# Kernel optimization log

Measured on AMD Instinct MI355X. Metric: run time of the kernel, lower is better.

Reference implementation:

```python
import jax, jax.numpy as jnp
import numpy as np

B, L, C, H = 4, 1024, 768, 12
D = C // H  # head_ch = 64


def setup_inputs() -> dict:
    key = jax.random.key(0)
    ks = jax.random.split(key, 8)
    s = 1.0 / np.sqrt(C)
    return {
        "inputs_q": jax.random.normal(ks[0], (B, L, C), jnp.float32),
        "inputs_kv": jax.random.normal(ks[1], (B, L, C), jnp.float32),
        "Wq": jax.random.normal(ks[2], (C, H * D), jnp.float32) * s,
        "Wk": jax.random.normal(ks[3], (C, H * D), jnp.float32) * s,
        "Wv": jax.random.normal(ks[4], (C, H * D), jnp.float32) * s,
        "Wout": jax.random.normal(ks[5], (H * D, C), jnp.float32) * s,
        "W_pre": jax.random.normal(ks[6], (H, H), jnp.float32) * (1.0 / np.sqrt(H)),
        "W_post": jax.random.normal(ks[7], (H, H), jnp.float32) * (1.0 / np.sqrt(H)),
    }


def reference(inputs_q, inputs_kv, Wq, Wk, Wv, Wout, W_pre, W_post):
    # Linear projections (no bias), split into heads: b l (h d) -> b h l d
    def split_heads(x):
        b, l, _ = x.shape
        return x.reshape(b, l, H, D).transpose(0, 2, 1, 3)

    q = split_heads(inputs_q @ Wq) / jnp.sqrt(jnp.asarray(D, inputs_q.dtype))
    k = split_heads(inputs_kv @ Wk)
    v = split_heads(inputs_kv @ Wv)

    # Attention logits [b, h, l, k]
    weights = jnp.einsum('bhld,bhkd->bhlk', q, k)
    # Talking-heads: learned cross-head mixing pre-softmax
    weights = jnp.einsum('bhlk,hi->bilk', weights, W_pre)
    weights = jax.nn.softmax(weights, axis=-1)
    # Talking-heads post-softmax mixing
    weights = jnp.einsum('bhlk,hi->bilk', weights, W_post)

    scores = jnp.einsum('bhlk,bhkd->bhld', weights, v)
    scores = scores.transpose(0, 2, 1, 3).reshape(B, L, H * D)  # b l (h d)
    return scores @ Wout
```

## Files before the change

kernel.cpp:

```cpp
#include <hip/hip_runtime.h>

#define BB 4
#define LL 1024
#define CC 768
#define HH 12
#define DD 64

typedef unsigned short ushort_t;
typedef __attribute__((ext_vector_type(8))) short bf16x8;
typedef __attribute__((ext_vector_type(4))) float f32x4;
typedef __attribute__((ext_vector_type(2))) float f32x2;

__device__ inline ushort_t f2bf(float x) {
    union { float f; unsigned u; } v; v.f = x;
    unsigned r = (v.u + 0x7FFFu + ((v.u >> 16) & 1u)) >> 16;
    return (ushort_t)r;
}
__device__ inline float bf2f(ushort_t u) {
    union { unsigned u; float f; } v; v.u = ((unsigned)u) << 16;
    return v.f;
}
__device__ inline float u2f(unsigned u) {
    union { unsigned u; float f; } v; v.u = u;
    return v.f;
}

__device__ inline void stage_rows(const ushort_t* __restrict__ g, int stride,
                                  ushort_t* lds, int nbytes, int wave, int lane) {
    const int ko = (lane & 3) << 3;
    const int rsub = lane >> 2;
    for (int off = wave * 1024; off < nbytes; off += 4096) {
        int row = (off >> 6) + rsub;
        __builtin_amdgcn_global_load_lds(
            (const __attribute__((address_space(1))) void*)(g + (size_t)row * stride + ko),
            (__attribute__((address_space(3))) void*)(lds + (off >> 1)),
            16, 0, 0);
    }
}

__global__ __launch_bounds__(256) void prep(const float* __restrict__ q, const float* __restrict__ kv,
                                            const float* __restrict__ w0, const float* __restrict__ w1,
                                            const float* __restrict__ w2, const float* __restrict__ w3,
                                            ushort_t* __restrict__ qo, ushort_t* __restrict__ kvo,
                                            ushort_t* __restrict__ o0, ushort_t* __restrict__ o1,
                                            ushort_t* __restrict__ o2, ushort_t* __restrict__ o3) {
    __shared__ float t[32][33];
    const int bx = blockIdx.x;
    if (bx < 3072) {
        const float* src = bx < 1536 ? q : kv;
        ushort_t* dst = bx < 1536 ? qo : kvo;
        int bb = bx < 1536 ? bx : bx - 1536;
        size_t i = ((size_t)bb * 256 + threadIdx.x) * 8;
        float4 a = *(const float4*)(src + i);
        float4 b = *(const float4*)(src + i + 4);
        ushort_t u[8] = {f2bf(a.x), f2bf(a.y), f2bf(a.z), f2bf(a.w),
                         f2bf(b.x), f2bf(b.y), f2bf(b.z), f2bf(b.w)};
        *(uint4*)(dst + i) = *(uint4*)u;
    } else {
        int w = bx - 3072;
        int z = w / 576, rem = w % 576;
        const float* W = z == 0 ? w0 : z == 1 ? w1 : z == 2 ? w2 : w3;
        ushort_t* Wt   = z == 0 ? o0 : z == 1 ? o1 : z == 2 ? o2 : o3;
        const int c = threadIdx.x & 31, r0 = threadIdx.x >> 5;
        const int kb = (rem / 24) * 32, nb = (rem % 24) * 32;
#pragma unroll
        for (int i = 0; i < 4; ++i)
            t[r0 + 8 * i][c] = W[(size_t)(kb + r0 + 8 * i) * CC + nb + c];
        __syncthreads();
#pragma unroll
        for (int i = 0; i < 4; ++i)
            Wt[(size_t)(nb + r0 + 8 * i) * CC + kb + c] = f2bf(t[c][r0 + 8 * i]);
    }
}

__global__ __launch_bounds__(256) void proj_gemm(const ushort_t* __restrict__ Aq,
                                                 const ushort_t* __restrict__ Akv,
                                                 const ushort_t* __restrict__ Wqt,
                                                 const ushort_t* __restrict__ Wkt,
                                                 const ushort_t* __restrict__ Wvt,
                                                 ushort_t* __restrict__ Qo,
                                                 ushort_t* __restrict__ Ko,
                                                 ushort_t* __restrict__ Vto) {
    const int z = blockIdx.z;
    const ushort_t* A  = (z == 0) ? Aq : Akv;
    const ushort_t* Wt = (z == 0) ? Wqt : (z == 1 ? Wkt : Wvt);

    __shared__ __align__(16) ushort_t a_lds[128 * 32];
    __shared__ __align__(16) ushort_t b_lds[128 * 32];

    const int tid = threadIdx.x;
    const int bm = blockIdx.x * 128, bn = blockIdx.y * 128;
    const int wave = tid >> 6, lane = tid & 63;
    const int quad = lane >> 4, lq = lane & 15;
    const int wr = wave >> 1, wc = wave & 1;

    f32x4 acc[4][4] = {};

    for (int k0 = 0; k0 < CC; k0 += 32) {
        stage_rows(A + (size_t)bm * CC + k0, CC, a_lds, 8192, wave, lane);
        stage_rows(Wt + (size_t)bn * CC + k0, CC, b_lds, 8192, wave, lane);
        __syncthreads();
        bf16x8 af[4], bfr[4];
#pragma unroll
        for (int mi = 0; mi < 4; ++mi)
            af[mi] = *(bf16x8*)&a_lds[(wr * 64 + mi * 16 + lq) * 32 + quad * 8];
#pragma unroll
        for (int ni = 0; ni < 4; ++ni)
            bfr[ni] = *(bf16x8*)&b_lds[(wc * 64 + ni * 16 + lq) * 32 + quad * 8];
#pragma unroll
        for (int mi = 0; mi < 4; ++mi)
#pragma unroll
            for (int ni = 0; ni < 4; ++ni)
                acc[mi][ni] = __builtin_amdgcn_mfma_f32_16x16x32_bf16(af[mi], bfr[ni], acc[mi][ni], 0, 0, 0);
        __syncthreads();
    }

    const float scale = (z == 0) ? 0.125f : 1.0f;
#pragma unroll
    for (int mi = 0; mi < 4; ++mi)
#pragma unroll
        for (int ni = 0; ni < 4; ++ni)
#pragma unroll
            for (int r = 0; r < 4; ++r) {
                int row = bm + wr * 64 + mi * 16 + quad * 4 + r;
                int col = bn + wc * 64 + ni * 16 + lq;
                int b = row >> 10, l = row & 1023, h = col >> 6, d = col & 63;
                ushort_t v = f2bf(acc[mi][ni][r] * scale);
                if (z == 0)      Qo[((size_t)(b * HH + h) * LL + l) * DD + d] = v;
                else if (z == 1) Ko[((size_t)(b * HH + h) * LL + l) * DD + d] = v;
                else             Vto[((size_t)(b * HH + h) * DD + d) * LL + l] = v;
            }
}

__global__ __launch_bounds__(256) void qk_gemm(const ushort_t* __restrict__ Q,
                                               const ushort_t* __restrict__ K,
                                               ushort_t* __restrict__ S) {
    __shared__ __align__(16) ushort_t a_lds[128 * 32];
    __shared__ __align__(16) ushort_t b_lds[128 * 32];

    const int tid = threadIdx.x;
    const int bm = blockIdx.x * 128, bn = blockIdx.y * 128;
    const int bh = blockIdx.z;
    const ushort_t* Qh = Q + (size_t)bh * LL * DD;
    const ushort_t* Kh = K + (size_t)bh * LL * DD;
    const int wave = tid >> 6, lane = tid & 63;
    const int quad = lane >> 4, lq = lane & 15;
    const int wr = wave >> 1, wc = wave & 1;

    f32x4 acc[4][4] = {};

    for (int k0 = 0; k0 < DD; k0 += 32) {
        stage_rows(Qh + (size_t)bm * DD + k0, DD, a_lds, 8192, wave, lane);
        stage_rows(Kh + (size_t)bn * DD + k0, DD, b_lds, 8192, wave, lane);
        __syncthreads();
        bf16x8 af[4], bfr[4];
#pragma unroll
        for (int mi = 0; mi < 4; ++mi)
            af[mi] = *(bf16x8*)&a_lds[(wr * 64 + mi * 16 + lq) * 32 + quad * 8];
#pragma unroll
        for (int ni = 0; ni < 4; ++ni)
            bfr[ni] = *(bf16x8*)&b_lds[(wc * 64 + ni * 16 + lq) * 32 + quad * 8];
#pragma unroll
        for (int mi = 0; mi < 4; ++mi)
#pragma unroll
            for (int ni = 0; ni < 4; ++ni)
                acc[mi][ni] = __builtin_amdgcn_mfma_f32_16x16x32_bf16(af[mi], bfr[ni], acc[mi][ni], 0, 0, 0);
        __syncthreads();
    }

#pragma unroll
    for (int mi = 0; mi < 4; ++mi)
#pragma unroll
        for (int ni = 0; ni < 4; ++ni)
#pragma unroll
            for (int r = 0; r < 4; ++r) {
                int row = bm + wr * 64 + mi * 16 + quad * 4 + r;
                int col = bn + wc * 64 + ni * 16 + lq;
                S[((size_t)bh * LL + row) * LL + col] = f2bf(acc[mi][ni][r]);
            }
}

__global__ __launch_bounds__(256) void mix_softmax(ushort_t* __restrict__ S,
                                                   const float* __restrict__ Wpre,
                                                   const float* __restrict__ Wpost) {
    __shared__ float reds[4][16];

    const int tid = threadIdx.x;
    const int wave = tid >> 6, lane = tid & 63;
    const int l = blockIdx.x, b = blockIdx.y;

    const size_t hstride = (size_t)LL * LL;
    const size_t base = ((size_t)(b * HH) * LL + l) * LL + tid * 4;

    f32x2 p[HH][2];
#pragma unroll
    for (int i = 0; i < HH; ++i) { p[i][0] = 0.f; p[i][1] = 0.f; }
#pragma unroll
    for (int h = 0; h < HH; ++h) {
        uint2 raw = *(const uint2*)&S[base + h * hstride];
        f32x2 v0, v1;
        v0.x = u2f(raw.x << 16); v0.y = u2f(raw.x & 0xFFFF0000u);
        v1.x = u2f(raw.y << 16); v1.y = u2f(raw.y & 0xFFFF0000u);
#pragma unroll
        for (int i = 0; i < HH; ++i) {
            float w = Wpre[h * HH + i];
            p[i][0] += v0 * w;
            p[i][1] += v1 * w;
        }
    }

    float sm[HH];
#pragma unroll
    for (int i = 0; i < HH; ++i) {
        p[i][0].x = __expf(p[i][0].x); p[i][0].y = __expf(p[i][0].y);
        p[i][1].x = __expf(p[i][1].x); p[i][1].y = __expf(p[i][1].y);
        f32x2 t2 = p[i][0] + p[i][1];
        float ss = t2.x + t2.y;
#pragma unroll
        for (int off = 32; off; off >>= 1) ss += __shfl_xor(ss, off);
        sm[i] = ss;
    }
    if (lane == 0) {
#pragma unroll
        for (int i = 0; i < HH; ++i) reds[wave][i] = sm[i];
    }
    __syncthreads();
#pragma unroll
    for (int i = 0; i < HH; ++i) {
        float tot = (reds[0][i] + reds[1][i]) + (reds[2][i] + reds[3][i]);
        float inv = 1.0f / tot;
        p[i][0] *= inv; p[i][1] *= inv;
    }

#pragma unroll
    for (int i = 0; i < HH; ++i) {
        f32x2 a0 = 0.f, a1 = 0.f;
#pragma unroll
        for (int h = 0; h < HH; ++h) {
            float w = Wpost[h * HH + i];
            a0 += p[h][0] * w;
            a1 += p[h][1] * w;
        }
        ushort_t u[4] = {f2bf(a0.x), f2bf(a0.y), f2bf(a1.x), f2bf(a1.y)};
        *(uint2*)&S[base + i * hstride] = *(uint2*)u;
    }
}

__global__ __launch_bounds__(256) void pv_gemm(const ushort_t* __restrict__ P,
                                               const ushort_t* __restrict__ Vt,
                                               ushort_t* __restrict__ att) {
    __shared__ __align__(16) ushort_t a_lds[64 * 32];
    __shared__ __align__(16) ushort_t b_lds[64 * 32];

    const int tid = threadIdx.x;
    const int bm = blockIdx.x * 64;
    const int bh = blockIdx.y;
    const int b = bh / HH, ih = bh % HH;
    const ushort_t* Ph = P + ((size_t)bh << 20);
    const ushort_t* Vh = Vt + (size_t)bh * LL * DD;
    const int wave = tid >> 6, lane = tid & 63;
    const int quad = lane >> 4, lq = lane & 15;
    const int wr = wave >> 1, wc = wave & 1;

    f32x4 acc[2][2] = {};

    for (int k0 = 0; k0 < LL; k0 += 32) {
        stage_rows(Ph + (size_t)bm * LL + k0, LL, a_lds, 4096, wave, lane);
        stage_rows(Vh + k0, LL, b_lds, 4096, wave, lane);
        __syncthreads();
        bf16x8 af[2], bfr[2];
#pragma unroll
        for (int mi = 0; mi < 2; ++mi)
            af[mi] = *(bf16x8*)&a_lds[(wr * 32 + mi * 16 + lq) * 32 + quad * 8];
#pragma unroll
        for (int ni = 0; ni < 2; ++ni)
            bfr[ni] = *(bf16x8*)&b_lds[(wc * 32 + ni * 16 + lq) * 32 + quad * 8];
#pragma unroll
        for (int mi = 0; mi < 2; ++mi)
#pragma unroll
            for (int ni = 0; ni < 2; ++ni)
                acc[mi][ni] = __builtin_amdgcn_mfma_f32_16x16x32_bf16(af[mi], bfr[ni], acc[mi][ni], 0, 0, 0);
        __syncthreads();
    }

#pragma unroll
    for (int mi = 0; mi < 2; ++mi)
#pragma unroll
        for (int ni = 0; ni < 2; ++ni)
#pragma unroll
            for (int r = 0; r < 4; ++r) {
                int lrow = bm + wr * 32 + mi * 16 + quad * 4 + r;
                int col = wc * 32 + ni * 16 + lq;
                att[((size_t)(b * LL) + lrow) * CC + ih * DD + col] = f2bf(acc[mi][ni][r]);
            }
}

__global__ __launch_bounds__(256) void out_gemm(const ushort_t* __restrict__ A,
                                                const ushort_t* __restrict__ Wt,
                                                float* __restrict__ out) {
    __shared__ __align__(16) ushort_t a_lds[128 * 32];
    __shared__ __align__(16) ushort_t b_lds[64 * 32];

    const int tid = threadIdx.x;
    const int bm = blockIdx.x * 128, bn = blockIdx.y * 64;
    const int wave = tid >> 6, lane = tid & 63;
    const int quad = lane >> 4, lq = lane & 15;
    const int wr = wave >> 1, wc = wave & 1;

    f32x4 acc[4][2] = {};

    for (int k0 = 0; k0 < CC; k0 += 32) {
        stage_rows(A + (size_t)bm * CC + k0, CC, a_lds, 8192, wave, lane);
        stage_rows(Wt + (size_t)bn * CC + k0, CC, b_lds, 4096, wave, lane);
        __syncthreads();
        bf16x8 af[4], bfr[2];
#pragma unroll
        for (int mi = 0; mi < 4; ++mi)
            af[mi] = *(bf16x8*)&a_lds[(wr * 64 + mi * 16 + lq) * 32 + quad * 8];
#pragma unroll
        for (int ni = 0; ni < 2; ++ni)
            bfr[ni] = *(bf16x8*)&b_lds[(wc * 32 + ni * 16 + lq) * 32 + quad * 8];
#pragma unroll
        for (int mi = 0; mi < 4; ++mi)
#pragma unroll
            for (int ni = 0; ni < 2; ++ni)
                acc[mi][ni] = __builtin_amdgcn_mfma_f32_16x16x32_bf16(af[mi], bfr[ni], acc[mi][ni], 0, 0, 0);
        __syncthreads();
    }

#pragma unroll
    for (int mi = 0; mi < 4; ++mi)
#pragma unroll
        for (int ni = 0; ni < 2; ++ni)
#pragma unroll
            for (int r = 0; r < 4; ++r) {
                int row = bm + wr * 64 + mi * 16 + quad * 4 + r;
                int col = bn + wc * 32 + ni * 16 + lq;
                out[(size_t)row * CC + col] = acc[mi][ni][r];
            }
}

extern "C" void kernel_launch(void* const* d_in, const int* in_sizes, int n_in,
                              void* d_out, int out_size, void* d_ws, size_t ws_size,
                              hipStream_t stream) {
    const float* inputs_q  = (const float*)d_in[0];
    const float* inputs_kv = (const float*)d_in[1];
    const float* Wq   = (const float*)d_in[2];
    const float* Wk   = (const float*)d_in[3];
    const float* Wv   = (const float*)d_in[4];
    const float* Wout = (const float*)d_in[5];
    const float* Wpre  = (const float*)d_in[6];
    const float* Wpost = (const float*)d_in[7];
    float* out = (float*)d_out;

    const size_t nS   = (size_t)BB * HH * LL * LL;
    const size_t nQKV = (size_t)BB * HH * LL * DD;
    const size_t nW   = (size_t)CC * CC;

    ushort_t* Sb   = (ushort_t*)d_ws;
    ushort_t* Qb   = Sb + nS;
    ushort_t* Kb   = Qb + nQKV;
    ushort_t* Vtb  = Kb + nQKV;
    ushort_t* attb = Vtb + nQKV;
    ushort_t* inq  = attb + nQKV;
    ushort_t* inkv = inq + nQKV;
    ushort_t* Wqt  = inkv + nQKV;
    ushort_t* Wkt  = Wqt + nW;
    ushort_t* Wvt  = Wkt + nW;
    ushort_t* Wot  = Wvt + nW;

    dim3 blk(256);

    prep<<<dim3(5376), blk, 0, stream>>>(inputs_q, inputs_kv, Wq, Wk, Wv, Wout,
                                         inq, inkv, Wqt, Wkt, Wvt, Wot);
    proj_gemm<<<dim3(32, 6, 3), blk, 0, stream>>>(inq, inkv, Wqt, Wkt, Wvt, Qb, Kb, Vtb);
    qk_gemm<<<dim3(8, 8, BB * HH), blk, 0, stream>>>(Qb, Kb, Sb);
    mix_softmax<<<dim3(LL, BB), blk, 0, stream>>>(Sb, Wpre, Wpost);
    pv_gemm<<<dim3(16, BB * HH), blk, 0, stream>>>(Sb, Vtb, attb);
    out_gemm<<<dim3(32, 12), blk, 0, stream>>>(attb, Wot, out);
}
```

Baseline: 233.7 us.

## Fuse QK with pre-mix/exp and PV with post-mix, dropping separate softmax pass

The QK GEMM now computes all 12 heads for a 32x32 tile, applies the pre-softmax head mixing and exp in registers, and writes head-interleaved exp values plus atomically accumulated row sums Z. A new PV kernel reads those values, normalises by 1/Z, applies post-softmax mixing on the fly, and runs the PV MFMAs from swizzled LDS tiles. This removes the standalone mix_softmax kernel and one full read-modify-write of the score tensor. In exchange it skips max-subtraction in softmax, which risks overflow, and it adds float atomics for Z, zeroed in prep.

```diff
diff --git a/kernel.cpp b/kernel.cpp
--- a/kernel.cpp
+++ b/kernel.cpp
@@ -1,4 +1,5 @@
 #include <hip/hip_runtime.h>
+#include <hip/hip_bf16.h>
 
 #define BB 4
 #define LL 1024
@@ -16,13 +17,14 @@
     unsigned r = (v.u + 0x7FFFu + ((v.u >> 16) & 1u)) >> 16;
     return (ushort_t)r;
 }
-__device__ inline float bf2f(ushort_t u) {
-    union { unsigned u; float f; } v; v.u = ((unsigned)u) << 16;
-    return v.f;
-}
 __device__ inline float u2f(unsigned u) {
     union { unsigned u; float f; } v; v.u = u;
     return v.f;
+}
+__device__ inline unsigned pack2bf(float lo, float hi) {
+    union { __hip_bfloat162 v; unsigned u; } r;
+    r.v = __float22bfloat162_rn(make_float2(lo, hi));
+    return r.u;
 }
 
 __device__ inline void stage_rows(const ushort_t* __restrict__ g, int stride,
@@ -43,7 +45,8 @@
                                             const float* __restrict__ w2, const float* __restrict__ w3,
                                             ushort_t* __restrict__ qo, ushort_t* __restrict__ kvo,
                                             ushort_t* __restrict__ o0, ushort_t* __restrict__ o1,
-                                            ushort_t* __restrict__ o2, ushort_t* __restrict__ o3) {
+                                            ushort_t* __restrict__ o2, ushort_t* __restrict__ o3,
+                                            float* __restrict__ Zp) {
     __shared__ float t[32][33];
     const int bx = blockIdx.x;
     if (bx < 3072) {
@@ -56,7 +59,7 @@
         ushort_t u[8] = {f2bf(a.x), f2bf(a.y), f2bf(a.z), f2bf(a.w),
                          f2bf(b.x), f2bf(b.y), f2bf(b.z), f2bf(b.w)};
         *(uint4*)(dst + i) = *(uint4*)u;
-    } else {
+    } else if (bx < 5376) {
         int w = bx - 3072;
         int z = w / 576, rem = w % 576;
         const float* W = z == 0 ? w0 : z == 1 ? w1 : z == 2 ? w2 : w3;
@@ -70,6 +73,8 @@
 #pragma unroll
         for (int i = 0; i < 4; ++i)
             Wt[(size_t)(nb + r0 + 8 * i) * CC + kb + c] = f2bf(t[c][r0 + 8 * i]);
+    } else {
+        Zp[(bx - 5376) * 256 + threadIdx.x] = 0.f;
     }
 }
 
@@ -132,167 +137,191 @@
             }
 }
 
-__global__ __launch_bounds__(256) void qk_gemm(const ushort_t* __restrict__ Q,
-                                               const ushort_t* __restrict__ K,
-                                               ushort_t* __restrict__ S) {
-    __shared__ __align__(16) ushort_t a_lds[128 * 32];
-    __shared__ __align__(16) ushort_t b_lds[128 * 32];
+__global__ __launch_bounds__(256) void qk_premix(const ushort_t* __restrict__ Q,
+                                                 const ushort_t* __restrict__ K,
+                                                 const float* __restrict__ Wpre,
+                                                 ushort_t* __restrict__ E,
+                                                 float* __restrict__ Z) {
+    __shared__ __align__(16) ushort_t k_lds[2][2048];
+    __shared__ __align__(16) ushort_t q_lds[2][2048];
 
     const int tid = threadIdx.x;
-    const int bm = blockIdx.x * 128, bn = blockIdx.y * 128;
-    const int bh = blockIdx.z;
-    const ushort_t* Qh = Q + (size_t)bh * LL * DD;
-    const ushort_t* Kh = K + (size_t)bh * LL * DD;
-    const int wave = tid >> 6, lane = tid & 63;
+    const int bk = blockIdx.x * 32;
+    const int bl = blockIdx.y * 32;
+    const int b  = blockIdx.z;
+    const int lane = tid & 63, wave = tid >> 6;
     const int quad = lane >> 4, lq = lane & 15;
     const int wr = wave >> 1, wc = wave & 1;
 
-    f32x4 acc[4][4] = {};
-
-    for (int k0 = 0; k0 < DD; k0 += 32) {
-        stage_rows(Qh + (size_t)bm * DD + k0, DD, a_lds, 8192, wave, lane);
-        stage_rows(Kh + (size_t)bn * DD + k0, DD, b_lds, 8192, wave, lane);
-        __syncthreads();
-        bf16x8 af[4], bfr[4];
-#pragma unroll
-        for (int mi = 0; mi < 4; ++mi)
-            af[mi] = *(bf16x8*)&a_lds[(wr * 64 + mi * 16 + lq) * 32 + quad * 8];
-#pragma unroll
-        for (int ni = 0; ni < 4; ++ni)
-            bfr[ni] = *(bf16x8*)&b_lds[(wc * 64 + ni * 16 + lq) * 32 + quad * 8];
-#pragma unroll
-        for (int mi = 0; mi < 4; ++mi)
-#pragma unroll
-            for (int ni = 0; ni < 4; ++ni)
-                acc[mi][ni] = __builtin_amdgcn_mfma_f32_16x16x32_bf16(af[mi], bfr[ni], acc[mi][ni], 0, 0, 0);
-        __syncthreads();
-    }
-
-#pragma unroll
-    for (int mi = 0; mi < 4; ++mi)
-#pragma unroll
-        for (int ni = 0; ni < 4; ++ni)
-#pragma unroll
-            for (int r = 0; r < 4; ++r) {
-                int row = bm + wr * 64 + mi * 16 + quad * 4 + r;
-                int col = bn + wc * 64 + ni * 16 + lq;
-                S[((size_t)bh * LL + row) * LL + col] = f2bf(acc[mi][ni][r]);
+    const int o = tid << 4;
+    const int goff = ((o >> 6) & 31) * DD + (o >> 11) * 32 + ((o >> 4) & 3) * 8;
+    const ushort_t* Kbase = K + ((size_t)b * HH * LL + bk) * DD;
+    const ushort_t* Qbase = Q + ((size_t)b * HH * LL + bl) * DD;
+
+    f32x4 acc[HH] = {};
+
+#define STAGE_QK(h, bf)                                                                             \
+    do {                                                                                            \
+        __builtin_amdgcn_global_load_lds(                                                           \
+            (const __attribute__((address_space(1))) void*)(Kbase + (size_t)(h) * LL * DD + goff),  \
+            (__attribute__((address_space(3))) void*)(&k_lds[bf][0] + (o >> 1)), 16, 0, 0);         \
+        __builtin_amdgcn_global_load_lds(                                                           \
+            (const __attribute__((address_space(1))) void*)(Qbase + (size_t)(h) * LL * DD + goff),  \
+            (__attribute__((address_space(3))) void*)(&q_lds[bf][0] + (o >> 1)), 16, 0, 0);         \
+    } while (0)
+
+    STAGE_QK(0, 0);
+    __syncthreads();
+#pragma unroll
+    for (int h = 0; h < HH; ++h) {
+        const int buf = h & 1;
+        if (h < HH - 1) STAGE_QK(h + 1, buf ^ 1);
+        bf16x8 a0 = *(bf16x8*)&k_lds[buf][(wr * 16 + lq) * 32 + quad * 8];
+        bf16x8 a1 = *(bf16x8*)&k_lds[buf][1024 + (wr * 16 + lq) * 32 + quad * 8];
+        bf16x8 b0 = *(bf16x8*)&q_lds[buf][(wc * 16 + lq) * 32 + quad * 8];
+        bf16x8 b1 = *(bf16x8*)&q_lds[buf][1024 + (wc * 16 + lq) * 32 + quad * 8];
+        acc[h] = __builtin_amdgcn_mfma_f32_16x16x32_bf16(a0, b0, acc[h], 0, 0, 0);
+        acc[h] = __builtin_amdgcn_mfma_f32_16x16x32_bf16(a1, b1, acc[h], 0, 0, 0);
+        __syncthreads();
+    }
+#undef STAGE_QK
+
+    unsigned pk[6][4];
+#pragma unroll
+    for (int i2 = 0; i2 < 6; ++i2) {
+        f32x4 m0 = {}, m1 = {};
+#pragma unroll
+        for (int h = 0; h < HH; ++h) {
+            m0 += acc[h] * Wpre[h * HH + 2 * i2];
+            m1 += acc[h] * Wpre[h * HH + 2 * i2 + 1];
+        }
+#pragma unroll
+        for (int r = 0; r < 4; ++r)
+            pk[i2][r] = pack2bf(__expf(m0[r]), __expf(m1[r]));
+    }
+
+    float zp[HH];
+#pragma unroll
+    for (int i2 = 0; i2 < 6; ++i2) {
+        float s0 = 0.f, s1 = 0.f;
+#pragma unroll
+        for (int r = 0; r < 4; ++r) {
+            s0 += u2f(pk[i2][r] << 16);
+            s1 += u2f(pk[i2][r] & 0xFFFF0000u);
+        }
+        zp[2 * i2] = s0; zp[2 * i2 + 1] = s1;
+    }
+#pragma unroll
+    for (int i = 0; i < HH; ++i) {
+        zp[i] += __shfl_xor(zp[i], 16);
+        zp[i] += __shfl_xor(zp[i], 32);
+    }
+    if (quad == 0) {
+#pragma unroll
+        for (int i = 0; i < HH; ++i)
+            atomicAdd(&Z[((size_t)b * HH + i) * LL + bl + wc * 16 + lq], zp[i]);
+    }
+
+#pragma unroll
+    for (int r = 0; r < 4; ++r) {
+        ushort_t* ep = E + (((size_t)b * LL + bk + wr * 16 + quad * 4 + r) * LL
+                            + bl + wc * 16 + lq) * HH;
+        *(uint2*)ep       = make_uint2(pk[0][r], pk[1][r]);
+        *(uint2*)(ep + 4) = make_uint2(pk[2][r], pk[3][r]);
+        *(uint2*)(ep + 8) = make_uint2(pk[4][r], pk[5][r]);
+    }
+}
+
+__global__ __launch_bounds__(512) void pv_postmix(const ushort_t* __restrict__ E,
+                                                  const ushort_t* __restrict__ Vt,
+                                                  const float* __restrict__ Wpost,
+                                                  const float* __restrict__ Z,
+                                                  ushort_t* __restrict__ att) {
+    __shared__ __align__(16) ushort_t v_lds[HH * 64 * 64];
+    __shared__ __align__(16) ushort_t p_lds[HH * 16 * 64];
+
+    const int tid = threadIdx.x;
+    const int bl = blockIdx.x * 16;
+    const int b  = blockIdx.y;
+    const int lane = tid & 63, wave = tid >> 6;
+    const int quad = lane >> 4, lq = lane & 15;
+    const int ig = (wave >> 2) * 6;
+    const int wd = wave & 3;
+    const int lmix = tid & 15, kp = tid >> 4;
+
+    float invZ[HH];
+#pragma unroll
+    for (int h = 0; h < HH; ++h)
+        invZ[h] = 1.0f / Z[((size_t)b * HH + h) * LL + bl + lmix];
+
+    f32x4 acc[6] = {};
+
+#pragma unroll 1
+    for (int kt = 0; kt < 16; ++kt) {
+#pragma unroll
+        for (int j = 0; j < 12; ++j) {
+            const int o = (tid << 4) + (j << 13);
+            const int row = o >> 7;
+            const int cs = ((o >> 4) & 7) ^ (row & 7);
+            const ushort_t* src = Vt + ((size_t)b * HH * 64 + row) * LL + kt * 64 + cs * 8;
+            __builtin_amdgcn_global_load_lds(
+                (const __attribute__((address_space(1))) void*)src,
+                (__attribute__((address_space(3))) void*)(v_lds + (o >> 1)), 16, 0, 0);
+        }
+
+        const int kg = kt * 64 + kp * 2;
+        const ushort_t* ep = E + (((size_t)b * LL + kg) * LL + bl + lmix) * HH;
+        uint2 ua = *(const uint2*)ep;
+        uint2 ub = *(const uint2*)(ep + 4);
+        uint2 uc = *(const uint2*)(ep + 8);
+        uint2 va = *(const uint2*)(ep + (size_t)LL * HH);
+        uint2 vb = *(const uint2*)(ep + (size_t)LL * HH + 4);
+        uint2 vc = *(const uint2*)(ep + (size_t)LL * HH + 8);
+        unsigned w0[6] = {ua.x, ua.y, ub.x, ub.y, uc.x, uc.y};
+        unsigned w1[6] = {va.x, va.y, vb.x, vb.y, vc.x, vc.y};
+
+        f32x2 m[HH] = {};
+#pragma unroll
+        for (int h2 = 0; h2 < 6; ++h2) {
+            f32x2 pe, po;
+            pe.x = u2f(w0[h2] << 16);           pe.y = u2f(w1[h2] << 16);
+            po.x = u2f(w0[h2] & 0xFFFF0000u);   po.y = u2f(w1[h2] & 0xFFFF0000u);
+            pe *= invZ[2 * h2];
+            po *= invZ[2 * h2 + 1];
+#pragma unroll
+            for (int i = 0; i < HH; ++i) {
+                m[i] += pe * Wpost[(2 * h2) * HH + i];
+                m[i] += po * Wpost[(2 * h2 + 1) * HH + i];
             }
-}
-
-__global__ __launch_bounds__(256) void mix_softmax(ushort_t* __restrict__ S,
-                                                   const float* __restrict__ Wpre,
-                                                   const float* __restrict__ Wpost) {
-    __shared__ float reds[4][16];
-
-    const int tid = threadIdx.x;
-    const int wave = tid >> 6, lane = tid & 63;
-    const int l = blockIdx.x, b = blockIdx.y;
-
-    const size_t hstride = (size_t)LL * LL;
-    const size_t base = ((size_t)(b * HH) * LL + l) * LL + tid * 4;
-
-    f32x2 p[HH][2];
-#pragma unroll
-    for (int i = 0; i < HH; ++i) { p[i][0] = 0.f; p[i][1] = 0.f; }
-#pragma unroll
-    for (int h = 0; h < HH; ++h) {
-        uint2 raw = *(const uint2*)&S[base + h * hstride];
-        f32x2 v0, v1;
-        v0.x = u2f(raw.x << 16); v0.y = u2f(raw.x & 0xFFFF0000u);
-        v1.x = u2f(raw.y << 16); v1.y = u2f(raw.y & 0xFFFF0000u);
-#pragma unroll
-        for (int i = 0; i < HH; ++i) {
-            float w = Wpre[h * HH + i];
-            p[i][0] += v0 * w;
-            p[i][1] += v1 * w;
         }
-    }
-
-    float sm[HH];
-#pragma unroll
-    for (int i = 0; i < HH; ++i) {
-        p[i][0].x = __expf(p[i][0].x); p[i][0].y = __expf(p[i][0].y);
-        p[i][1].x = __expf(p[i][1].x); p[i][1].y = __expf(p[i][1].y);
-        f32x2 t2 = p[i][0] + p[i][1];
-        float ss = t2.x + t2.y;
-#pragma unroll
-        for (int off = 32; off; off >>= 1) ss += __shfl_xor(ss, off);
-        sm[i] = ss;
-    }
-    if (lane == 0) {
-#pragma unroll
-        for (int i = 0; i < HH; ++i) reds[wave][i] = sm[i];
-    }
-    __syncthreads();
-#pragma unroll
-    for (int i = 0; i < HH; ++i) {
-        float tot = (reds[0][i] + reds[1][i]) + (reds[2][i] + reds[3][i]);
-        float inv = 1.0f / tot;
-        p[i][0] *= inv; p[i][1] *= inv;
-    }
-
-#pragma unroll
-    for (int i = 0; i < HH; ++i) {
-        f32x2 a0 = 0.f, a1 = 0.f;
-#pragma unroll
-        for (int h = 0; h < HH; ++h) {
-            float w = Wpost[h * HH + i];
-            a0 += p[h][0] * w;
-            a1 += p[h][1] * w;
+        {
+            const int cs = (kp >> 2) ^ (lmix & 7);
+            unsigned* pw = (unsigned*)p_lds;
+#pragma unroll
+            for (int i = 0; i < HH; ++i)
+                pw[(i * 16 + lmix) * 32 + cs * 4 + (kp & 3)] = pack2bf(m[i].x, m[i].y);
         }
-        ushort_t u[4] = {f2bf(a0.x), f2bf(a0.y), f2bf(a1.x), f2bf(a1.y)};
-        *(uint2*)&S[base + i * hstride] = *(uint2*)u;
-    }
-}
-
-__global__ __launch_bounds__(256) void pv_gemm(const ushort_t* __restrict__ P,
-                                               const ushort_t* __restrict__ Vt,
-                                               ushort_t* __restrict__ att) {
-    __shared__ __align__(16) ushort_t a_lds[64 * 32];
-    __shared__ __align__(16) ushort_t b_lds[64 * 32];
-
-    const int tid = threadIdx.x;
-    const int bm = blockIdx.x * 64;
-    const int bh = blockIdx.y;
-    const int b = bh / HH, ih = bh % HH;
-    const ushort_t* Ph = P + ((size_t)bh << 20);
-    const ushort_t* Vh = Vt + (size_t)bh * LL * DD;
-    const int wave = tid >> 6, lane = tid & 63;
-    const int quad = lane >> 4, lq = lane & 15;
-    const int wr = wave >> 1, wc = wave & 1;
-
-    f32x4 acc[2][2] = {};
-
-    for (int k0 = 0; k0 < LL; k0 += 32) {
-        stage_rows(Ph + (size_t)bm * LL + k0, LL, a_lds, 4096, wave, lane);
-        stage_rows(Vh + k0, LL, b_lds, 4096, wave, lane);
-        __syncthreads();
-        bf16x8 af[2], bfr[2];
-#pragma unroll
-        for (int mi = 0; mi < 2; ++mi)
-            af[mi] = *(bf16x8*)&a_lds[(wr * 32 + mi * 16 + lq) * 32 + quad * 8];
-#pragma unroll
-        for (int ni = 0; ni < 2; ++ni)
-            bfr[ni] = *(bf16x8*)&b_lds[(wc * 32 + ni * 16 + lq) * 32 + quad * 8];
-#pragma unroll
-        for (int mi = 0; mi < 2; ++mi)
-#pragma unroll
-            for (int ni = 0; ni < 2; ++ni)
-                acc[mi][ni] = __builtin_amdgcn_mfma_f32_16x16x32_bf16(af[mi], bfr[ni], acc[mi][ni], 0, 0, 0);
-        __syncthreads();
-    }
-
-#pragma unroll
-    for (int mi = 0; mi < 2; ++mi)
-#pragma unroll
-        for (int ni = 0; ni < 2; ++ni)
-#pragma unroll
-            for (int r = 0; r < 4; ++r) {
-                int lrow = bm + wr * 32 + mi * 16 + quad * 4 + r;
-                int col = wc * 32 + ni * 16 + lq;
-                att[((size_t)(b * LL) + lrow) * CC + ih * DD + col] = f2bf(acc[mi][ni][r]);
+        __syncthreads();
+
+#pragma unroll
+        for (int k0 = 0; k0 < 2; ++k0)
+#pragma unroll
+            for (int ii = 0; ii < 6; ++ii) {
+                const int hh = ig + ii;
+                const int ch = ((k0 << 2) + quad) ^ (lq & 7);
+                bf16x8 pa  = *(bf16x8*)&p_lds[(hh * 16 + lq) * 64 + ch * 8];
+                bf16x8 vbf = *(bf16x8*)&v_lds[(hh * 64 + wd * 16 + lq) * 64 + ch * 8];
+                acc[ii] = __builtin_amdgcn_mfma_f32_16x16x32_bf16(pa, vbf, acc[ii], 0, 0, 0);
             }
+        __syncthreads();
+    }
+
+#pragma unroll
+    for (int ii = 0; ii < 6; ++ii)
+#pragma unroll
+        for (int r = 0; r < 4; ++r)
+            att[((size_t)b * LL + bl + quad * 4 + r) * CC + (ig + ii) * 64 + wd * 16 + lq] =
+                f2bf(acc[ii][r]);
 }
 
 __global__ __launch_bounds__(256) void out_gemm(const ushort_t* __restrict__ A,
@@ -357,8 +386,8 @@
     const size_t nQKV = (size_t)BB * HH * LL * DD;
     const size_t nW   = (size_t)CC * CC;
 
-    ushort_t* Sb   = (ushort_t*)d_ws;
-    ushort_t* Qb   = Sb + nS;
+    ushort_t* Eb   = (ushort_t*)d_ws;
+    ushort_t* Qb   = Eb + nS;
     ushort_t* Kb   = Qb + nQKV;
     ushort_t* Vtb  = Kb + nQKV;
     ushort_t* attb = Vtb + nQKV;
@@ -368,14 +397,14 @@
     ushort_t* Wkt  = Wqt + nW;
     ushort_t* Wvt  = Wkt + nW;
     ushort_t* Wot  = Wvt + nW;
+    float*    Zb   = (float*)(Wot + nW);
 
     dim3 blk(256);
 
-    prep<<<dim3(5376), blk, 0, stream>>>(inputs_q, inputs_kv, Wq, Wk, Wv, Wout,
-                                         inq, inkv, Wqt, Wkt, Wvt, Wot);
+    prep<<<dim3(5568), blk, 0, stream>>>(inputs_q, inputs_kv, Wq, Wk, Wv, Wout,
+                                         inq, inkv, Wqt, Wkt, Wvt, Wot, Zb);
     proj_gemm<<<dim3(32, 6, 3), blk, 0, stream>>>(inq, inkv, Wqt, Wkt, Wvt, Qb, Kb, Vtb);
-    qk_gemm<<<dim3(8, 8, BB * HH), blk, 0, stream>>>(Qb, Kb, Sb);
-    mix_softmax<<<dim3(LL, BB), blk, 0, stream>>>(Sb, Wpre, Wpost);
-    pv_gemm<<<dim3(16, BB * HH), blk, 0, stream>>>(Sb, Vtb, attb);
+    qk_premix<<<dim3(32, 32, BB), blk, 0, stream>>>(Qb, Kb, Wpre, Eb, Zb);
+    pv_postmix<<<dim3(LL / 16, BB), dim3(512), 0, stream>>>(Eb, Vtb, Wpost, Zb, attb);
     out_gemm<<<dim3(32, 12), blk, 0, stream>>>(attb, Wot, out);
 }
```

Result: slower. 261.5 us (+11.9%).
